# Kernel tuning notes

Hardware: AMD Instinct MI355X
Metric: run time of the kernel (lower is better)

The kernel has to match this reference:

```python
import jax, jax.numpy as jnp
import numpy as np

T, B, D = 512, 32, 1024


def setup_inputs() -> dict:
    key = jax.random.key(0)
    kx, kwh, kwx, kwg = jax.random.split(key, 4)
    x = jax.random.normal(kx, (T, B, D), dtype=jnp.float32)
    # W_h: orthogonal init scaled by 0.5
    a = jax.random.normal(kwh, (D, D), dtype=jnp.float32)
    q, r = jnp.linalg.qr(a)
    W_h = 0.5 * q * jnp.sign(jnp.diag(r))[None, :]
    # xavier uniform for W_x, W_g: bound = sqrt(6/(D+D))
    bound = float(np.sqrt(6.0 / (D + D)))
    W_x = jax.random.uniform(kwx, (D, D), minval=-bound, maxval=bound, dtype=jnp.float32)
    W_g = jax.random.uniform(kwg, (D, D), minval=-bound, maxval=bound, dtype=jnp.float32)
    b = jnp.zeros((D,), dtype=jnp.float32)
    b_g = jnp.zeros((D,), dtype=jnp.float32)
    return {"x": x, "W_h": W_h, "W_x": W_x, "W_g": W_g, "b": b, "b_g": b_g}


def reference(x, W_h, W_x, W_g, b, b_g):
    # x: [T, B, D]
    Tn, Bn, Dn = x.shape
    # Precompute input projections (batched over T*B, like the torch code)
    Wx_all = jnp.einsum('tbd,ed->tbe', x, W_x)                      # [T,B,D]
    gate_all = jax.nn.sigmoid(jnp.einsum('tbd,ed->tbe', x, W_g) + b_g)  # [T,B,D]
    h0 = jnp.zeros((Bn, Dn), dtype=x.dtype)

    def step(h_prev, inp):
        wx_t, g_t = inp
        pre_act = h_prev @ W_h.T + wx_t + b
        h_new = h_prev + g_t * jnp.tanh(pre_act)
        out_t = h_new * jax.nn.silu(h_new)
        return h_new, (h_new, out_t)

    _, (h_seq, output) = jax.lax.scan(step, h0, (Wx_all, gate_all))
    h = jnp.concatenate([h0[None], h_seq], axis=0)  # [T+1,B,D]
    return output, h
```

## Files before the change

kernel.cpp:

```cpp
#include <hip/hip_runtime.h>
#include <hip/hip_bf16.h>
#include <stdint.h>


#define T_DIM 512
#define B_DIM 32
#define D_DIM 1024
#define M_DIM (T_DIM*B_DIM)

typedef __attribute__((ext_vector_type(4))) float f32x4;
typedef __attribute__((ext_vector_type(8))) short bf16x8;

__device__ inline unsigned short f2b(float f){
  union { float f; uint32_t u; } c; c.f = f;
  uint32_t u = c.u + 0x7fffu + ((c.u >> 16) & 1u);
  return (unsigned short)(u >> 16);
}
__device__ inline float b2f(unsigned short h){
  union { uint32_t u; float f; } c; c.u = ((uint32_t)h) << 16;
  return c.f;
}

__global__ void init_kernel(float* __restrict__ out_h0,
                            float* __restrict__ h_ex,
                            uint32_t* __restrict__ flags){
  int i = blockIdx.x*blockDim.x + threadIdx.x;
  out_h0[i] = 0.f;
  int g = i >> 12, j = i & 4095;
  h_ex[(size_t)g*8192 + j] = 0.f;
  if (i < 4096) flags[i] = 0;
}

template<int MODE>
__global__ __launch_bounds__(256, 2)
void proj_m(const float* __restrict__ X, const float* __restrict__ W,
            const float* __restrict__ bias, float* __restrict__ OUT)
{
  __shared__ unsigned short Ah[128*64];
  __shared__ unsigned short Al[128*64];
  __shared__ unsigned short Bh[128*64];
  __shared__ unsigned short Bl[128*64];
  char* AhB=(char*)Ah; char* AlB=(char*)Al; char* BhB=(char*)Bh; char* BlB=(char*)Bl;
  const int tid  = threadIdx.x;
  const int lane = tid & 63;
  const int wave = tid >> 6;
  const int m0 = blockIdx.y * 128;
  const int n0 = blockIdx.x * 128;
  const int wm = (wave >> 1) * 64;
  const int wn = (wave & 1) * 64;
  const int fr = lane & 15;
  const int fq = lane >> 4;

  f32x4 acc[4][4];
  #pragma unroll
  for (int i=0;i<4;++i)
    #pragma unroll
    for (int j=0;j<4;++j) acc[i][j] = (f32x4){0.f,0.f,0.f,0.f};

  for (int kt = 0; kt < D_DIM/64; ++kt) {
    #pragma unroll
    for (int c = 0; c < 4; ++c) {
      int idx = tid + c*256;
      int row = idx >> 3;
      int k8  = idx & 7;
      const float* ga = X + (size_t)(m0+row)*D_DIM + kt*64 + k8*8;
      const float* gb = W + (size_t)(n0+row)*D_DIM + kt*64 + k8*8;
      f32x4 a0 = *(const f32x4*)ga, a1 = *(const f32x4*)(ga+4);
      f32x4 b0 = *(const f32x4*)gb, b1 = *(const f32x4*)(gb+4);
      bf16x8 vah, val, vbh, vbl;
      #pragma unroll
      for (int j=0;j<4;++j){
        unsigned short h;
        h = f2b(a0[j]); vah[j]   = (short)h; val[j]   = (short)f2b(a0[j]-b2f(h));
        h = f2b(a1[j]); vah[4+j] = (short)h; val[4+j] = (short)f2b(a1[j]-b2f(h));
        h = f2b(b0[j]); vbh[j]   = (short)h; vbl[j]   = (short)f2b(b0[j]-b2f(h));
        h = f2b(b1[j]); vbh[4+j] = (short)h; vbl[4+j] = (short)f2b(b1[j]-b2f(h));
      }
      int lb = row*128 + ((k8*16) ^ ((row&7)<<4));
      *(bf16x8*)(AhB + lb) = vah;
      *(bf16x8*)(AlB + lb) = val;
      *(bf16x8*)(BhB + lb) = vbh;
      *(bf16x8*)(BlB + lb) = vbl;
    }
    __syncthreads();
    #pragma unroll
    for (int kk=0; kk<2; ++kk) {
      bf16x8 afh[4], afl[4], bfh[4], bfl[4];
      #pragma unroll
      for (int i=0;i<4;++i){
        int row = wm+i*16+fr;
        int off = row*128 + ((kk*64 + fq*16) ^ ((row&7)<<4));
        afh[i] = *(const bf16x8*)(AhB + off);
        afl[i] = *(const bf16x8*)(AlB + off);
      }
      #pragma unroll
      for (int j=0;j<4;++j){
        int row = wn+j*16+fr;
        int off = row*128 + ((kk*64 + fq*16) ^ ((row&7)<<4));
        bfh[j] = *(const bf16x8*)(BhB + off);
        bfl[j] = *(const bf16x8*)(BlB + off);
      }
      #pragma unroll
      for (int i=0;i<4;++i)
        #pragma unroll
        for (int j=0;j<4;++j){
          acc[i][j] = __builtin_amdgcn_mfma_f32_16x16x32_bf16(afh[i], bfh[j], acc[i][j], 0,0,0);
          acc[i][j] = __builtin_amdgcn_mfma_f32_16x16x32_bf16(afh[i], bfl[j], acc[i][j], 0,0,0);
          acc[i][j] = __builtin_amdgcn_mfma_f32_16x16x32_bf16(afl[i], bfh[j], acc[i][j], 0,0,0);
        }
    }
    __syncthreads();
  }
  #pragma unroll
  for (int j=0;j<4;++j) {
    int col = n0 + wn + j*16 + fr;
    float bv = bias[col];
    #pragma unroll
    for (int i=0;i<4;++i) {
      int rowb = m0 + wm + i*16 + fq*4;
      #pragma unroll
      for (int r=0;r<4;++r) {
        float v = acc[i][j][r] + bv;
        if (MODE==1) v = 1.f/(1.f + expf(-v));
        OUT[(size_t)(rowb+r)*D_DIM + col] = v;
      }
    }
  }
}

__global__ __launch_bounds__(256, 1)
void rnn_persist(const float* __restrict__ Wh,
                 float* PO,
                 float* PH,
                 float* __restrict__ h_ex,
                 uint32_t* __restrict__ flags)
{
  __shared__ char  hsb[4*4096];
  __shared__ float part[16*137];

  const int tid = threadIdx.x;
  const int blk = blockIdx.x;
  const int g   = blk & 7;
  const int sl  = blk >> 3;
  const int e0  = sl * 32;
  const int b0  = g * 4;
  const int e2  = tid & 15;
  const int kc  = tid >> 4;

  f32x4 wh0[16], wh1[16];
  {
    const f32x4* wp0 = (const f32x4*)(Wh + (size_t)(e0 + 2*e2 + 0)*D_DIM + kc*64);
    const f32x4* wp1 = (const f32x4*)(Wh + (size_t)(e0 + 2*e2 + 1)*D_DIM + kc*64);
    #pragma unroll
    for (int i = 0; i < 16; ++i) { wh0[i] = wp0[i]; wh1[i] = wp1[i]; }
  }

  const int bl = tid >> 5;
  const int el = tid & 31;
  float hold = 0.f;

  for (int t = 0; t < T_DIM; ++t) {
    size_t idx_out = (size_t)t*32768 + (size_t)(b0 + bl)*D_DIM + e0 + el;
    float Pv = 0.f, Gv = 0.f;
    if (tid < 128) {
      Pv = PH[idx_out + 32768];
      Gv = PO[idx_out];
    }

    if (t > 0 && tid < 32) {
      const uint32_t* fp = flags + (size_t)(g*32 + tid)*16;
      while (__hip_atomic_load(fp, __ATOMIC_RELAXED, __HIP_MEMORY_SCOPE_AGENT)
             < (uint32_t)t)
        __builtin_amdgcn_s_sleep(1);
    }
    __syncthreads();

    {
      const char* hsrc = (const char*)(h_ex + (size_t)(g*2 + (t&1))*4096) + tid*16;
      f32x4 r0, r1, r2, r3;
      asm volatile("global_load_dwordx4 %0, %1, off sc0 sc1"
                   : "=v"(r0) : "v"(hsrc)          : "memory");
      asm volatile("global_load_dwordx4 %0, %1, off sc0 sc1"
                   : "=v"(r1) : "v"(hsrc + 4096)   : "memory");
      asm volatile("global_load_dwordx4 %0, %1, off sc0 sc1"
                   : "=v"(r2) : "v"(hsrc + 8192)   : "memory");
      asm volatile("global_load_dwordx4 %0, %1, off sc0 sc1"
                   : "=v"(r3) : "v"(hsrc + 12288)  : "memory");
      asm volatile("s_waitcnt vmcnt(0)" ::: "memory");
      __builtin_amdgcn_sched_barrier(0);
      #pragma unroll
      for (int i = 0; i < 4; ++i) {
        int G   = i*256 + tid;
        int bq  = G >> 8;
        int g16 = G & 255;
        int g16s = g16 ^ (g16 >> 4);
        f32x4 v = (i==0) ? r0 : (i==1) ? r1 : (i==2) ? r2 : r3;
        *(f32x4*)(hsb + bq*4096 + g16s*16) = v;
      }
    }
    __syncthreads();

    float acc[4][2];
    #pragma unroll
    for (int b = 0; b < 4; ++b) { acc[b][0] = 0.f; acc[b][1] = 0.f; }
    #pragma unroll
    for (int i = 0; i < 16; ++i) {
      f32x4 w0 = wh0[i], w1 = wh1[i];
      #pragma unroll
      for (int b = 0; b < 4; ++b) {
        f32x4 hv = *(const f32x4*)(hsb + b*4096 + kc*256 + ((i ^ kc) << 4));
        float d0 = hv[0]*w0[0] + hv[1]*w0[1] + hv[2]*w0[2] + hv[3]*w0[3];
        float d1 = hv[0]*w1[0] + hv[1]*w1[1] + hv[2]*w1[2] + hv[3]*w1[3];
        acc[b][0] += d0;
        acc[b][1] += d1;
      }
    }
    #pragma unroll
    for (int b = 0; b < 4; ++b) {
      part[kc*137 + b*32 + 2*e2 + 0] = acc[b][0];
      part[kc*137 + b*32 + 2*e2 + 1] = acc[b][1];
    }
    __syncthreads();

    if (tid < 128) {
      float pre = 0.f;
      #pragma unroll
      for (int q = 0; q < 16; ++q) pre += part[q*137 + bl*32 + el];
      pre += Pv;
      float th = tanhf(pre);
      float hn = hold + Gv*th;
      hold = hn;
      float sg = 1.f/(1.f + expf(-hn));
      PO[idx_out] = hn*hn*sg;
      PH[idx_out + 32768] = hn;
      float* hdst = h_ex + (size_t)(g*2 + ((t+1)&1))*4096 + bl*1024 + e0 + el;
      asm volatile("global_store_dword %0, %1, off sc0 sc1"
                   :: "v"(hdst), "v"(hn) : "memory");
    }
    asm volatile("s_waitcnt vmcnt(0)" ::: "memory");
    __syncthreads();

    if (tid == 0) {
      uint32_t fv = (uint32_t)(t+1);
      uint32_t* fptr = flags + (size_t)(g*32 + sl)*16;
      asm volatile("global_store_dword %0, %1, off sc0 sc1"
                   :: "v"(fptr), "v"(fv) : "memory");
    }
  }
}

extern "C" void kernel_launch(void* const* d_in, const int* in_sizes, int n_in,
                              void* d_out, int out_size, void* d_ws, size_t ws_size,
                              hipStream_t stream) {
  const float* x  = (const float*)d_in[0];
  const float* Wh = (const float*)d_in[1];
  const float* Wx = (const float*)d_in[2];
  const float* Wg = (const float*)d_in[3];
  const float* b  = (const float*)d_in[4];
  const float* bg = (const float*)d_in[5];

  float* out_o = (float*)d_out;
  float* out_h = out_o + (size_t)M_DIM*D_DIM;

  char* ws = (char*)d_ws;
  float*    h_ex  = (float*)ws;
  uint32_t* flags = (uint32_t*)(ws + (256<<10));

  init_kernel<<<128, 256, 0, stream>>>(out_h, h_ex, flags);
  proj_m<1><<<dim3(8,128), 256, 0, stream>>>(x, Wg, bg, out_o);
  proj_m<0><<<dim3(8,128), 256, 0, stream>>>(x, Wx, b,  out_h + 32768);
  rnn_persist<<<256, 256, 0, stream>>>(Wh, out_o, out_h, h_ex, flags);
}
```

Measured before the change: 1.889 ms.

## Reshape recurrent matvec thread mapping to 8 outputs per thread with finer K split

```diff
diff --git a/kernel.cpp b/kernel.cpp
--- a/kernel.cpp
+++ b/kernel.cpp
@@ -128,6 +128,9 @@
   }
 }
 
+#define PART_EL 67
+#define PART_B  (32*PART_EL)
+
 __global__ __launch_bounds__(256, 1)
 void rnn_persist(const float* __restrict__ Wh,
                  float* PO,
@@ -136,7 +139,7 @@
                  uint32_t* __restrict__ flags)
 {
   __shared__ char  hsb[4*4096];
-  __shared__ float part[16*137];
+  __shared__ float part[4*PART_B];
 
   const int tid = threadIdx.x;
   const int blk = blockIdx.x;
@@ -144,15 +147,15 @@
   const int sl  = blk >> 3;
   const int e0  = sl * 32;
   const int b0  = g * 4;
-  const int e2  = tid & 15;
-  const int kc  = tid >> 4;
-
-  f32x4 wh0[16], wh1[16];
-  {
-    const f32x4* wp0 = (const f32x4*)(Wh + (size_t)(e0 + 2*e2 + 0)*D_DIM + kc*64);
-    const f32x4* wp1 = (const f32x4*)(Wh + (size_t)(e0 + 2*e2 + 1)*D_DIM + kc*64);
-    #pragma unroll
-    for (int i = 0; i < 16; ++i) { wh0[i] = wp0[i]; wh1[i] = wp1[i]; }
+  const int eq  = tid & 3;
+  const int kc  = tid >> 2;
+
+  f32x4 whr[8][4];
+  #pragma unroll
+  for (int e = 0; e < 8; ++e) {
+    const f32x4* wp = (const f32x4*)(Wh + (size_t)(e0 + eq*8 + e)*D_DIM + kc*16);
+    #pragma unroll
+    for (int i = 0; i < 4; ++i) whr[e][i] = wp[i];
   }
 
   const int bl = tid >> 5;
@@ -169,23 +172,23 @@
 
     if (t > 0 && tid < 32) {
       const uint32_t* fp = flags + (size_t)(g*32 + tid)*16;
-      while (__hip_atomic_load(fp, __ATOMIC_RELAXED, __HIP_MEMORY_SCOPE_AGENT)
-             < (uint32_t)t)
+      uint32_t v;
+      while (true) {
+        asm volatile("global_load_dword %0, %1, off sc0 sc1" : "=v"(v) : "v"(fp) : "memory");
+        asm volatile("s_waitcnt vmcnt(0)" ::: "memory");
+        if (v >= (uint32_t)t) break;
         __builtin_amdgcn_s_sleep(1);
+      }
     }
     __syncthreads();
 
     {
       const char* hsrc = (const char*)(h_ex + (size_t)(g*2 + (t&1))*4096) + tid*16;
       f32x4 r0, r1, r2, r3;
-      asm volatile("global_load_dwordx4 %0, %1, off sc0 sc1"
-                   : "=v"(r0) : "v"(hsrc)          : "memory");
-      asm volatile("global_load_dwordx4 %0, %1, off sc0 sc1"
-                   : "=v"(r1) : "v"(hsrc + 4096)   : "memory");
-      asm volatile("global_load_dwordx4 %0, %1, off sc0 sc1"
-                   : "=v"(r2) : "v"(hsrc + 8192)   : "memory");
-      asm volatile("global_load_dwordx4 %0, %1, off sc0 sc1"
-                   : "=v"(r3) : "v"(hsrc + 12288)  : "memory");
+      asm volatile("global_load_dwordx4 %0, %1, off sc0 sc1" : "=v"(r0) : "v"(hsrc)         : "memory");
+      asm volatile("global_load_dwordx4 %0, %1, off sc0 sc1" : "=v"(r1) : "v"(hsrc + 4096)  : "memory");
+      asm volatile("global_load_dwordx4 %0, %1, off sc0 sc1" : "=v"(r2) : "v"(hsrc + 8192)  : "memory");
+      asm volatile("global_load_dwordx4 %0, %1, off sc0 sc1" : "=v"(r3) : "v"(hsrc + 12288) : "memory");
       asm volatile("s_waitcnt vmcnt(0)" ::: "memory");
       __builtin_amdgcn_sched_barrier(0);
       #pragma unroll
@@ -200,32 +203,36 @@
     }
     __syncthreads();
 
-    float acc[4][2];
-    #pragma unroll
-    for (int b = 0; b < 4; ++b) { acc[b][0] = 0.f; acc[b][1] = 0.f; }
-    #pragma unroll
-    for (int i = 0; i < 16; ++i) {
-      f32x4 w0 = wh0[i], w1 = wh1[i];
+    float acc[4][8];
+    #pragma unroll
+    for (int b = 0; b < 4; ++b)
+      #pragma unroll
+      for (int e = 0; e < 8; ++e) acc[b][e] = 0.f;
+    #pragma unroll
+    for (int i = 0; i < 4; ++i) {
+      int gsw = ((kc*4 + i) ^ (kc >> 2)) << 4;
       #pragma unroll
       for (int b = 0; b < 4; ++b) {
-        f32x4 hv = *(const f32x4*)(hsb + b*4096 + kc*256 + ((i ^ kc) << 4));
-        float d0 = hv[0]*w0[0] + hv[1]*w0[1] + hv[2]*w0[2] + hv[3]*w0[3];
-        float d1 = hv[0]*w1[0] + hv[1]*w1[1] + hv[2]*w1[2] + hv[3]*w1[3];
-        acc[b][0] += d0;
-        acc[b][1] += d1;
-      }
-    }
-    #pragma unroll
-    for (int b = 0; b < 4; ++b) {
-      part[kc*137 + b*32 + 2*e2 + 0] = acc[b][0];
-      part[kc*137 + b*32 + 2*e2 + 1] = acc[b][1];
-    }
+        f32x4 hv = *(const f32x4*)(hsb + b*4096 + gsw);
+        #pragma unroll
+        for (int e = 0; e < 8; ++e) {
+          f32x4 w = whr[e][i];
+          acc[b][e] += hv[0]*w[0] + hv[1]*w[1] + hv[2]*w[2] + hv[3]*w[3];
+        }
+      }
+    }
+    #pragma unroll
+    for (int b = 0; b < 4; ++b)
+      #pragma unroll
+      for (int e = 0; e < 8; ++e)
+        part[b*PART_B + (eq*8 + e)*PART_EL + kc] = acc[b][e];
     __syncthreads();
 
     if (tid < 128) {
+      const float* pp = part + bl*PART_B + el*PART_EL;
       float pre = 0.f;
       #pragma unroll
-      for (int q = 0; q < 16; ++q) pre += part[q*137 + bl*32 + el];
+      for (int q = 0; q < 64; ++q) pre += pp[q];
       pre += Pv;
       float th = tanhf(pre);
       float hn = hold + Gv*th;
@@ -234,8 +241,7 @@
       PO[idx_out] = hn*hn*sg;
       PH[idx_out + 32768] = hn;
       float* hdst = h_ex + (size_t)(g*2 + ((t+1)&1))*4096 + bl*1024 + e0 + el;
-      asm volatile("global_store_dword %0, %1, off sc0 sc1"
-                   :: "v"(hdst), "v"(hn) : "memory");
+      asm volatile("global_store_dword %0, %1, off sc0 sc1" :: "v"(hdst), "v"(hn) : "memory");
     }
     asm volatile("s_waitcnt vmcnt(0)" ::: "memory");
     __syncthreads();
@@ -243,8 +249,7 @@
     if (tid == 0) {
       uint32_t fv = (uint32_t)(t+1);
       uint32_t* fptr = flags + (size_t)(g*32 + sl)*16;
-      asm volatile("global_store_dword %0, %1, off sc0 sc1"
-                   :: "v"(fptr), "v"(fv) : "memory");
+      asm volatile("global_store_dword %0, %1, off sc0 sc1" :: "v"(fptr), "v"(fv) : "memory");
     }
   }
 }
```

Result: slower. 2.106 ms (+11.5%).

## Replace flag-based step barrier with step-tagged hidden state exchange

Applied to the files above, without the earlier changes.

```diff
diff --git a/kernel.cpp b/kernel.cpp
--- a/kernel.cpp
+++ b/kernel.cpp
@@ -9,7 +9,10 @@
 #define M_DIM (T_DIM*B_DIM)
 
 typedef __attribute__((ext_vector_type(4))) float f32x4;
+typedef __attribute__((ext_vector_type(2))) float f32x2;
+typedef __attribute__((ext_vector_type(4))) int   i32x4;
 typedef __attribute__((ext_vector_type(8))) short bf16x8;
+typedef unsigned long long u64;
 
 __device__ inline unsigned short f2b(float f){
   union { float f; uint32_t u; } c; c.f = f;
@@ -20,15 +23,15 @@
   union { uint32_t u; float f; } c; c.u = ((uint32_t)h) << 16;
   return c.f;
 }
-
-__global__ void init_kernel(float* __restrict__ out_h0,
-                            float* __restrict__ h_ex,
-                            uint32_t* __restrict__ flags){
+__device__ inline float asf(int i){
+  union { int i; float f; } c; c.i = i; return c.f;
+}
+
+__global__ void init_kernel(float* __restrict__ out_h0, u64* __restrict__ h_ex){
   int i = blockIdx.x*blockDim.x + threadIdx.x;
   out_h0[i] = 0.f;
   int g = i >> 12, j = i & 4095;
-  h_ex[(size_t)g*8192 + j] = 0.f;
-  if (i < 4096) flags[i] = 0;
+  h_ex[(size_t)g*8192 + j] = 0ull;
 }
 
 template<int MODE>
@@ -128,12 +131,14 @@
   }
 }
 
+#define LOAD_TAGGED(r, off) \
+  asm volatile("global_load_dwordx4 %0, %1, off sc0 sc1" : "=v"(r) : "v"(hsrc + (off)) : "memory")
+
 __global__ __launch_bounds__(256, 1)
 void rnn_persist(const float* __restrict__ Wh,
                  float* PO,
                  float* PH,
-                 float* __restrict__ h_ex,
-                 uint32_t* __restrict__ flags)
+                 u64* __restrict__ h_ex)
 {
   __shared__ char  hsb[4*4096];
   __shared__ float part[16*137];
@@ -167,35 +172,33 @@
       Gv = PO[idx_out];
     }
 
-    if (t > 0 && tid < 32) {
-      const uint32_t* fp = flags + (size_t)(g*32 + tid)*16;
-      while (__hip_atomic_load(fp, __ATOMIC_RELAXED, __HIP_MEMORY_SCOPE_AGENT)
-             < (uint32_t)t)
-        __builtin_amdgcn_s_sleep(1);
-    }
-    __syncthreads();
-
     {
       const char* hsrc = (const char*)(h_ex + (size_t)(g*2 + (t&1))*4096) + tid*16;
-      f32x4 r0, r1, r2, r3;
-      asm volatile("global_load_dwordx4 %0, %1, off sc0 sc1"
-                   : "=v"(r0) : "v"(hsrc)          : "memory");
-      asm volatile("global_load_dwordx4 %0, %1, off sc0 sc1"
-                   : "=v"(r1) : "v"(hsrc + 4096)   : "memory");
-      asm volatile("global_load_dwordx4 %0, %1, off sc0 sc1"
-                   : "=v"(r2) : "v"(hsrc + 8192)   : "memory");
-      asm volatile("global_load_dwordx4 %0, %1, off sc0 sc1"
-                   : "=v"(r3) : "v"(hsrc + 12288)  : "memory");
-      asm volatile("s_waitcnt vmcnt(0)" ::: "memory");
+      i32x4 r0, r1, r2, r3, r4, r5, r6, r7;
+      const int expt = t;
+      while (true) {
+        LOAD_TAGGED(r0, 0);     LOAD_TAGGED(r1, 4096);
+        LOAD_TAGGED(r2, 8192);  LOAD_TAGGED(r3, 12288);
+        LOAD_TAGGED(r4, 16384); LOAD_TAGGED(r5, 20480);
+        LOAD_TAGGED(r6, 24576); LOAD_TAGGED(r7, 28672);
+        asm volatile("s_waitcnt vmcnt(0)" ::: "memory");
+        bool ok = (r0[1]==expt) & (r0[3]==expt) & (r1[1]==expt) & (r1[3]==expt)
+                & (r2[1]==expt) & (r2[3]==expt) & (r3[1]==expt) & (r3[3]==expt)
+                & (r4[1]==expt) & (r4[3]==expt) & (r5[1]==expt) & (r5[3]==expt)
+                & (r6[1]==expt) & (r6[3]==expt) & (r7[1]==expt) & (r7[3]==expt);
+        if (ok) break;
+        __builtin_amdgcn_s_sleep(1);
+      }
       __builtin_amdgcn_sched_barrier(0);
       #pragma unroll
-      for (int i = 0; i < 4; ++i) {
-        int G   = i*256 + tid;
-        int bq  = G >> 8;
-        int g16 = G & 255;
+      for (int j = 0; j < 8; ++j) {
+        i32x4 r = (j==0)?r0:(j==1)?r1:(j==2)?r2:(j==3)?r3:(j==4)?r4:(j==5)?r5:(j==6)?r6:r7;
+        int b   = j >> 1;
+        int ep  = (j&1)*512 + 2*tid;
+        int g16 = ep >> 2;
         int g16s = g16 ^ (g16 >> 4);
-        f32x4 v = (i==0) ? r0 : (i==1) ? r1 : (i==2) ? r2 : r3;
-        *(f32x4*)(hsb + bq*4096 + g16s*16) = v;
+        f32x2 v; v[0] = asf(r[0]); v[1] = asf(r[2]);
+        *(f32x2*)(hsb + b*4096 + g16s*16 + ((ep & 3) << 2)) = v;
       }
     }
     __syncthreads();
@@ -233,18 +236,11 @@
       float sg = 1.f/(1.f + expf(-hn));
       PO[idx_out] = hn*hn*sg;
       PH[idx_out + 32768] = hn;
-      float* hdst = h_ex + (size_t)(g*2 + ((t+1)&1))*4096 + bl*1024 + e0 + el;
-      asm volatile("global_store_dword %0, %1, off sc0 sc1"
-                   :: "v"(hdst), "v"(hn) : "memory");
-    }
-    asm volatile("s_waitcnt vmcnt(0)" ::: "memory");
-    __syncthreads();
-
-    if (tid == 0) {
-      uint32_t fv = (uint32_t)(t+1);
-      uint32_t* fptr = flags + (size_t)(g*32 + sl)*16;
-      asm volatile("global_store_dword %0, %1, off sc0 sc1"
-                   :: "v"(fptr), "v"(fv) : "memory");
+      union { float f; uint32_t u; } cb; cb.f = hn;
+      u64 pk = (u64)cb.u | ((u64)(uint32_t)(t+1) << 32);
+      u64* hdst = h_ex + (size_t)(g*2 + ((t+1)&1))*4096 + (size_t)bl*1024 + e0 + el;
+      asm volatile("global_store_dwordx2 %0, %1, off sc0 sc1"
+                   :: "v"(hdst), "v"(pk) : "memory");
     }
   }
 }
@@ -262,12 +258,10 @@
   float* out_o = (float*)d_out;
   float* out_h = out_o + (size_t)M_DIM*D_DIM;
 
-  char* ws = (char*)d_ws;
-  float*    h_ex  = (float*)ws;
-  uint32_t* flags = (uint32_t*)(ws + (256<<10));
-
-  init_kernel<<<128, 256, 0, stream>>>(out_h, h_ex, flags);
+  u64* h_ex = (u64*)d_ws;
+
+  init_kernel<<<128, 256, 0, stream>>>(out_h, h_ex);
   proj_m<1><<<dim3(8,128), 256, 0, stream>>>(x, Wg, bg, out_o);
   proj_m<0><<<dim3(8,128), 256, 0, stream>>>(x, Wx, b,  out_h + 32768);
-  rnn_persist<<<256, 256, 0, stream>>>(Wh, out_o, out_h, h_ex, flags);
-}
+  rnn_persist<<<256, 256, 0, stream>>>(Wh, out_o, out_h, h_ex);
+}
```

Measured after the change: 2.297 ms. +21.6%, slower.
